# Performance work log

Measured on AMD Instinct MI355X. Metric: run time of the kernel, lower is better.

Reference implementation:

```python
import jax, jax.numpy as jnp
import numpy as np
from jax import lax

B = 8192
NUM_EXPERTS = 5
TOP_K = 3
NUM_CLASSES = 10
FEAT = 5 * 5 * 64  # 1600, flatten dim after conv stack on 28x28x1


def _conv(x, w, b):
    # NHWC input, HWIO kernel, VALID padding, stride 1
    y = lax.conv_general_dilated(x, w, (1, 1), 'VALID',
                                 dimension_numbers=('NHWC', 'HWIO', 'NHWC'))
    return y + b


def _maxpool2(x):
    return lax.reduce_window(x, -jnp.inf, lax.max,
                             (1, 2, 2, 1), (1, 2, 2, 1), 'VALID')


def setup_inputs() -> dict:
    key = jax.random.key(0)
    ks = jax.random.split(key, 8)
    x = jax.random.normal(ks[0], (B, 28, 28, 1), dtype=jnp.float32)
    # conv kernels: glorot-ish small init
    conv1_w = jax.random.normal(ks[1], (3, 3, 1, 32), dtype=jnp.float32) * 0.1
    conv1_b = jnp.zeros((32,), jnp.float32)
    conv2_w = jax.random.normal(ks[2], (3, 3, 32, 64), dtype=jnp.float32) * 0.05
    conv2_b = jnp.zeros((64,), jnp.float32)
    # gating + experts use RandomNormal(stddev=0.001), zero bias per source
    gate_w = jax.random.normal(ks[3], (FEAT, NUM_EXPERTS), dtype=jnp.float32) * 0.001
    gate_b = jnp.zeros((NUM_EXPERTS,), jnp.float32)
    exp_w = jax.random.normal(ks[4], (NUM_EXPERTS, FEAT, NUM_CLASSES), dtype=jnp.float32) * 0.001
    exp_b = jnp.zeros((NUM_EXPERTS, NUM_CLASSES), jnp.float32)
    return {'x': x, 'conv1_w': conv1_w, 'conv1_b': conv1_b,
            'conv2_w': conv2_w, 'conv2_b': conv2_b,
            'gate_w': gate_w, 'gate_b': gate_b,
            'exp_w': exp_w, 'exp_b': exp_b}


def reference(x, conv1_w, conv1_b, conv2_w, conv2_b, gate_w, gate_b, exp_w, exp_b):
    # conv backbone (dropout is identity at inference)
    h = jax.nn.relu(_conv(x, conv1_w, conv1_b))        # [B,26,26,32]
    h = _maxpool2(h)                                   # [B,13,13,32]
    h = jax.nn.relu(_conv(h, conv2_w, conv2_b))        # [B,11,11,64]
    h = _maxpool2(h)                                   # [B,5,5,64]
    feat = h.reshape(h.shape[0], -1)                   # [B,1600]

    # gating: softmax over experts, then top-k
    gates = jax.nn.softmax(feat @ gate_w + gate_b)     # [B,E]
    top_w, top_idx = lax.top_k(gates, TOP_K)           # [B,K], [B,K]

    # all-expert outputs (E small), gather the selected ones, weighted combine
    all_out = jnp.einsum('bd,edh->beh', feat, exp_w) + exp_b   # [B,E,C]
    top_out = jnp.take_along_axis(all_out, top_idx[:, :, None], axis=1)  # [B,K,C]
    combined = jnp.einsum('bkh,bk->bh', top_out, top_w)        # [B,C]

    return jax.nn.softmax(combined)
```

## Files before the change

kernel.cpp:

```cpp
#include <hip/hip_runtime.h>
#include <hip/hip_bf16.h>

#define BLOCK 512
#define IPB 4
#define EIPB 16
#define FB_STRIDE 1616
#define ES_STRIDE 1608
#define H1_STRIDE 40

#define W2T_OFF 0
#define EWT_OFF 18432
#define W1C_OFF 120832
#define WS_SHORTS 121856
#define FEAT_OFF 121856

typedef __attribute__((ext_vector_type(8))) short short8;
typedef __attribute__((ext_vector_type(4))) float f32x4;

#define SEL_LO 0x05040100u
#define SEL_HI 0x07060302u

static __device__ __forceinline__ unsigned short f2bf(float f) {
    unsigned int u = __builtin_bit_cast(unsigned int, f);
    u = (u + 0x7FFFu + ((u >> 16) & 1u)) >> 16;
    return (unsigned short)u;
}
static __device__ __forceinline__ float bf2f(unsigned short h) {
    unsigned int u = ((unsigned int)h) << 16;
    return __builtin_bit_cast(float, u);
}
static __device__ __forceinline__ unsigned int pack_hl(float v) {
    const unsigned short h = f2bf(v);
    const unsigned short l = f2bf(v - bf2f(h));
    return (unsigned int)h | ((unsigned int)l << 16);
}
static __device__ __forceinline__ unsigned int pkbf2(float a, float b) {
    return (unsigned int)f2bf(a) | ((unsigned int)f2bf(b) << 16);
}

__global__ void moe_prep(const float* __restrict__ w2, const float* __restrict__ gw,
                         const float* __restrict__ ew, const float* __restrict__ w1,
                         unsigned short* __restrict__ ws) {
    int i = blockIdx.x * 256 + threadIdx.x;
    if (i < 18432) {
        int kpos = i >> 11, rem = i & 2047, oc = rem >> 5, j = rem & 31;
        int ic = ((j & 1) << 4) | (j >> 1);
        ws[W2T_OFF + i] = f2bf(w2[(kpos * 32 + ic) * 64 + oc]);
    }
    int j2 = i - EWT_OFF;
    if (j2 >= 0 && j2 < 102400) {
        int ks = j2 >> 11, rem = j2 & 2047, n = rem >> 5, k = rem & 31;
        int kk = ks * 32 + k;
        int wv = kk >> 6, jj = kk & 63;
        int r = jj & 31;
        int oc = ((jj >> 5) << 5) | ((r & 1) << 4) | (r >> 1);
        int d = wv * 64 + oc;
        float v = 0.f;
        if (n < 50)      v = ew[(n / 10) * 16000 + d * 10 + (n % 10)];
        else if (n < 55) v = gw[d * 5 + (n - 50)];
        ws[EWT_OFF + j2] = f2bf(v);
    }
    int p = i - W1C_OFF;
    if (p >= 0 && p < 1024) {
        int n = p >> 5, k = p & 31;
        unsigned short val = 0;
        if (k < 27) {
            int t = (k < 9) ? k : (k < 18 ? k - 9 : k - 18);
            float w = w1[t * 32 + n];
            unsigned short hi = f2bf(w);
            val = (k >= 9 && k < 18) ? f2bf(w - bf2f(hi)) : hi;
        }
        ws[W1C_OFF + p] = val;
    }
}

__global__ __launch_bounds__(BLOCK, 4)
void moe_conv(const float* __restrict__ x, const float* __restrict__ b1,
              const float* __restrict__ b2, const unsigned short* __restrict__ ws,
              unsigned short* __restrict__ feat, int B)
{
    __shared__ unsigned int xsp[2][784];
    __shared__ __align__(16) unsigned short h1p[2][169 * H1_STRIDE];
    __shared__ float b1s[32];
    __shared__ float b2s[64];

    const int tid  = threadIdx.x;
    const int wid  = tid >> 6;
    const int lane = tid & 63;
    const int l15  = lane & 15;
    const int lg   = lane >> 4;

    if (tid < 32) b1s[tid] = b1[tid];
    if (tid < 64) b2s[tid] = b2[tid];

    const int mt0 = wid >> 1;
    const int n0  = (wid & 1) * 2;
    short8 bfA[9], bfB[9];
    #pragma unroll
    for (int kp = 0; kp < 9; kp++) {
        bfA[kp] = *(const short8*)&ws[W2T_OFF + (kp * 64 + n0 * 16 + l15) * 32 + lg * 8];
        bfB[kp] = *(const short8*)&ws[W2T_OFF + (kp * 64 + (n0 + 1) * 16 + l15) * 32 + lg * 8];
    }
    const short8 c1f0 = *(const short8*)&ws[W1C_OFF + l15 * 32 + lg * 8];
    const short8 c1f1 = *(const short8*)&ws[W1C_OFF + (16 + l15) * 32 + lg * 8];

    const int img0 = blockIdx.x * IPB;
    {
        int im = img0 < B ? img0 : B - 1;
        const float* xg = x + (size_t)im * 784;
        xsp[0][tid] = pack_hl(xg[tid]);
        if (tid + BLOCK < 784) xsp[0][tid + BLOCK] = pack_hl(xg[tid + BLOCK]);
    }
    __syncthreads();

    #pragma unroll
    for (int p = 0; p <= IPB; ++p) {
        const bool do_c1 = (p < IPB);
        const bool do_c2 = (p >= 1);
        const bool pre   = (p + 1 < IPB);

        float f0 = 0.f, f1 = 0.f;
        if (pre) {
            int im2 = img0 + p + 1; if (im2 >= B) im2 = B - 1;
            const float* xg2 = x + (size_t)im2 * 784;
            f0 = xg2[tid];
            if (tid + BLOCK < 784) f1 = xg2[tid + BLOCK];
        }

        if (do_c2) {
            const int it = p - 1;
            const int img = img0 + it;
            const unsigned short* h1cur = h1p[it & 1];
            unsigned short* frow = feat + (size_t)img * 1600;
            #pragma unroll
            for (int mi = 0; mi < 2; ++mi) {
                const int mt = mt0 + mi * 4;
                const int m = mt * 16 + l15;
                int wsrc = m >> 2; if (wsrc > 24) wsrc = 24;
                const int s = m & 3;
                const int cy = 2 * (wsrc / 5) + (s >> 1);
                const int cx = 2 * (wsrc % 5) + (s & 1);
                const char* abase = (const char*)h1cur + (cy * 13 + cx) * (H1_STRIDE * 2) + lg * 16;
                f32x4 a0 = {0.f, 0.f, 0.f, 0.f};
                f32x4 a1 = {0.f, 0.f, 0.f, 0.f};
                #pragma unroll
                for (int ky = 0; ky < 3; ky++) {
                    #pragma unroll
                    for (int kx = 0; kx < 3; kx++) {
                        const short8 af = *(const short8*)(abase + (ky * 13 + kx) * (H1_STRIDE * 2));
                        a0 = __builtin_amdgcn_mfma_f32_16x16x32_bf16(af, bfA[ky * 3 + kx], a0, 0, 0, 0);
                        a1 = __builtin_amdgcn_mfma_f32_16x16x32_bf16(af, bfB[ky * 3 + kx], a1, 0, 0, 0);
                    }
                }
                const int wv = mt * 4 + lg;
                if (wv < 25 && img < B) {
                    const int oc0 = n0 * 16 + l15;
                    const float m0 = fmaxf(fmaxf(a0.x, a0.y), fmaxf(a0.z, a0.w)) + b2s[oc0];
                    const float m1 = fmaxf(fmaxf(a1.x, a1.y), fmaxf(a1.z, a1.w)) + b2s[oc0 + 16];
                    *(unsigned int*)&frow[wv * 64 + ((n0 >> 1) << 5) + 2 * l15] =
                        pkbf2(fmaxf(m0, 0.f), fmaxf(m1, 0.f));
                }
            }
        }

        if (do_c1) {
            const unsigned int* xcur = xsp[p & 1];
            unsigned short* h1dst = h1p[p & 1];
            for (int mt = wid; mt < 43; mt += 8) {
                int wsrc = mt * 4 + (l15 >> 2); if (wsrc > 168) wsrc = 168;
                const int s  = l15 & 3;
                const int cy = 2 * (wsrc / 13) + (s >> 1);
                const int cx = 2 * (wsrc % 13) + (s & 1);
                const unsigned int* xb = &xcur[cy * 28 + cx];
                const unsigned int t0 = xb[0],  t1 = xb[1],  t2 = xb[2];
                const unsigned int t3 = xb[28], t4 = xb[29], t5 = xb[30];
                const unsigned int t6 = xb[56], t7 = xb[57], t8 = xb[58];
                unsigned int a0, a1, a2, a3;
                if (lg == 0)      { a0 = __builtin_amdgcn_perm(t1, t0, SEL_LO);
                                    a1 = __builtin_amdgcn_perm(t3, t2, SEL_LO);
                                    a2 = __builtin_amdgcn_perm(t5, t4, SEL_LO);
                                    a3 = __builtin_amdgcn_perm(t7, t6, SEL_LO); }
                else if (lg == 1) { a0 = __builtin_amdgcn_perm(t0, t8, SEL_LO);
                                    a1 = __builtin_amdgcn_perm(t2, t1, SEL_LO);
                                    a2 = __builtin_amdgcn_perm(t4, t3, SEL_LO);
                                    a3 = __builtin_amdgcn_perm(t6, t5, SEL_LO); }
                else if (lg == 2) { a0 = __builtin_amdgcn_perm(t8, t7, SEL_LO);
                                    a1 = __builtin_amdgcn_perm(t1, t0, SEL_HI);
                                    a2 = __builtin_amdgcn_perm(t3, t2, SEL_HI);
                                    a3 = __builtin_amdgcn_perm(t5, t4, SEL_HI); }
                else              { a0 = __builtin_amdgcn_perm(t7, t6, SEL_HI);
                                    a1 = (t8 >> 16); a2 = 0u; a3 = 0u; }
                const uint4 av = make_uint4(a0, a1, a2, a3);
                const short8 af = __builtin_bit_cast(short8, av);
                f32x4 p0 = {0.f, 0.f, 0.f, 0.f};
                f32x4 p1 = {0.f, 0.f, 0.f, 0.f};
                p0 = __builtin_amdgcn_mfma_f32_16x16x32_bf16(af, c1f0, p0, 0, 0, 0);
                p1 = __builtin_amdgcn_mfma_f32_16x16x32_bf16(af, c1f1, p1, 0, 0, 0);
                const int window = mt * 4 + lg;
                if (window < 169) {
                    const float m0 = fmaxf(fmaxf(p0.x, p0.y), fmaxf(p0.z, p0.w)) + b1s[l15];
                    const float m1 = fmaxf(fmaxf(p1.x, p1.y), fmaxf(p1.z, p1.w)) + b1s[16 + l15];
                    *(unsigned int*)&h1dst[window * H1_STRIDE + 2 * l15] =
                        pkbf2(fmaxf(m0, 0.f), fmaxf(m1, 0.f));
                }
            }
        }

        if (pre) {
            xsp[(p + 1) & 1][tid] = pack_hl(f0);
            if (tid + BLOCK < 784) xsp[(p + 1) & 1][tid + BLOCK] = pack_hl(f1);
        }
        __syncthreads();
    }
}

__global__ __launch_bounds__(BLOCK, 2)
void moe_expert(const unsigned short* __restrict__ ws, const float* __restrict__ gb,
                const float* __restrict__ eb, float* __restrict__ out, int B)
{
    __shared__ __align__(16) unsigned short featS[EIPB * ES_STRIDE];
    __shared__ float allC[2][EIPB][64];

    const int tid  = threadIdx.x;
    const int wid  = tid >> 6;
    const int lane = tid & 63;
    const int l15  = lane & 15;
    const int lg   = lane >> 4;

    const unsigned short* feat = ws + FEAT_OFF;
    const unsigned short* ewt  = ws + EWT_OFF;
    const int img0 = blockIdx.x * EIPB;

    for (int i = tid; i < EIPB * 800; i += BLOCK) {
        const int r = i / 800, c = i - r * 800;
        const int img = img0 + r;
        unsigned int v = 0u;
        if (img < B) v = *(const unsigned int*)&feat[(size_t)img * 1600 + 2 * c];
        *(unsigned int*)&featS[r * ES_STRIDE + 2 * c] = v;
    }
    __syncthreads();

    {
        const int kh  = wid >> 2;
        const int ntE = wid & 3;
        const int bc  = ntE * 16 + l15;
        f32x4 acc = {0.f, 0.f, 0.f, 0.f};
        const int ks0 = kh * 25;
        for (int ks = ks0; ks < ks0 + 25; ++ks) {
            const short8 af = *(const short8*)&featS[l15 * ES_STRIDE + ks * 32 + lg * 8];
            const short8 bf = *(const short8*)&ewt[(ks * 64 + bc) * 32 + lg * 8];
            acc = __builtin_amdgcn_mfma_f32_16x16x32_bf16(af, bf, acc, 0, 0, 0);
        }
        const int r0 = lg * 4;
        allC[kh][r0 + 0][bc] = acc.x;
        allC[kh][r0 + 1][bc] = acc.y;
        allC[kh][r0 + 2][bc] = acc.z;
        allC[kh][r0 + 3][bc] = acc.w;
    }
    __syncthreads();

    if (tid < EIPB) {
        const int img = img0 + tid;
        if (img < B) {
            float gv[5], mx = -1e30f;
            #pragma unroll
            for (int g = 0; g < 5; g++) {
                gv[g] = allC[0][tid][50 + g] + allC[1][tid][50 + g] + gb[g];
                mx = fmaxf(mx, gv[g]);
            }
            float ssum = 0.f;
            #pragma unroll
            for (int g = 0; g < 5; g++) { gv[g] = expf(gv[g] - mx); ssum += gv[g]; }
            const float inv = 1.f / ssum;
            #pragma unroll
            for (int g = 0; g < 5; g++) gv[g] *= inv;

            int idx0, idx1, idx2; float wv0, wv1, wv2;
            unsigned usedMask = 0;
            {
                int bi = 0; float bv = -1e30f;
                #pragma unroll
                for (int g = 0; g < 5; g++)
                    if (gv[g] > bv) { bv = gv[g]; bi = g; }
                idx0 = bi; wv0 = bv; usedMask |= (1u << bi);
            }
            {
                int bi = 0; float bv = -1e30f;
                #pragma unroll
                for (int g = 0; g < 5; g++)
                    if (!(usedMask & (1u << g)) && gv[g] > bv) { bv = gv[g]; bi = g; }
                idx1 = bi; wv1 = bv; usedMask |= (1u << bi);
            }
            {
                int bi = 0; float bv = -1e30f;
                #pragma unroll
                for (int g = 0; g < 5; g++)
                    if (!(usedMask & (1u << g)) && gv[g] > bv) { bv = gv[g]; bi = g; }
                idx2 = bi; wv2 = bv;
            }
            float comb[10];
            #pragma unroll
            for (int cc = 0; cc < 10; cc++) {
                comb[cc] = wv0 * (allC[0][tid][idx0 * 10 + cc] + allC[1][tid][idx0 * 10 + cc] + eb[idx0 * 10 + cc])
                         + wv1 * (allC[0][tid][idx1 * 10 + cc] + allC[1][tid][idx1 * 10 + cc] + eb[idx1 * 10 + cc])
                         + wv2 * (allC[0][tid][idx2 * 10 + cc] + allC[1][tid][idx2 * 10 + cc] + eb[idx2 * 10 + cc]);
            }
            float m2 = -1e30f;
            #pragma unroll
            for (int cc = 0; cc < 10; cc++) m2 = fmaxf(m2, comb[cc]);
            float e[10], s2 = 0.f;
            #pragma unroll
            for (int cc = 0; cc < 10; cc++) { e[cc] = expf(comb[cc] - m2); s2 += e[cc]; }
            const float inv2 = 1.f / s2;
            #pragma unroll
            for (int cc = 0; cc < 10; cc++) out[(size_t)img * 10 + cc] = e[cc] * inv2;
        }
    }
}

__global__ __launch_bounds__(BLOCK, 3)
void moe_main_fused(const float* __restrict__ x, const float* __restrict__ b1,
                    const float* __restrict__ b2, const float* __restrict__ gb,
                    const float* __restrict__ eb, const unsigned short* __restrict__ ws,
                    float* __restrict__ out, int B)
{
    __shared__ unsigned int xsp[2][784];
    __shared__ __align__(16) unsigned short h1p[2][169 * H1_STRIDE];
    __shared__ __align__(16) unsigned short featbuf[IPB * FB_STRIDE];
    __shared__ float b1s[32];
    __shared__ float b2s[64];
    __shared__ float allC[2][IPB * 56];

    const int tid  = threadIdx.x;
    const int wid  = tid >> 6;
    const int lane = tid & 63;
    const int l15  = lane & 15;
    const int lg   = lane >> 4;

    if (tid < 32) b1s[tid] = b1[tid];
    if (tid < 64) b2s[tid] = b2[tid];

    const int mt0 = wid >> 1;
    const int n0  = (wid & 1) * 2;
    short8 bfA[9], bfB[9];
    #pragma unroll
    for (int kp = 0; kp < 9; kp++) {
        bfA[kp] = *(const short8*)&ws[W2T_OFF + (kp * 64 + n0 * 16 + l15) * 32 + lg * 8];
        bfB[kp] = *(const short8*)&ws[W2T_OFF + (kp * 64 + (n0 + 1) * 16 + l15) * 32 + lg * 8];
    }
    const short8 c1f0 = *(const short8*)&ws[W1C_OFF + l15 * 32 + lg * 8];
    const short8 c1f1 = *(const short8*)&ws[W1C_OFF + (16 + l15) * 32 + lg * 8];

    const int img0 = blockIdx.x * IPB;
    {
        int im = img0 < B ? img0 : B - 1;
        const float* xg = x + (size_t)im * 784;
        xsp[0][tid] = pack_hl(xg[tid]);
        if (tid + BLOCK < 784) xsp[0][tid + BLOCK] = pack_hl(xg[tid + BLOCK]);
    }
    __syncthreads();

    #pragma unroll
    for (int p = 0; p <= IPB; ++p) {
        const bool do_c1 = (p < IPB);
        const bool do_c2 = (p >= 1);
        const bool pre   = (p + 1 < IPB);

        float f0 = 0.f, f1 = 0.f;
        if (pre) {
            int im2 = img0 + p + 1; if (im2 >= B) im2 = B - 1;
            const float* xg2 = x + (size_t)im2 * 784;
            f0 = xg2[tid];
            if (tid + BLOCK < 784) f1 = xg2[tid + BLOCK];
        }

        if (do_c2) {
            const int it = p - 1;
            const unsigned short* h1cur = h1p[it & 1];
            #pragma unroll
            for (int mi = 0; mi < 2; ++mi) {
                const int mt = mt0 + mi * 4;
                const int m = mt * 16 + l15;
                int wsrc = m >> 2; if (wsrc > 24) wsrc = 24;
                const int s = m & 3;
                const int cy = 2 * (wsrc / 5) + (s >> 1);
                const int cx = 2 * (wsrc % 5) + (s & 1);
                const char* abase = (const char*)h1cur + (cy * 13 + cx) * (H1_STRIDE * 2) + lg * 16;
                f32x4 a0 = {0.f, 0.f, 0.f, 0.f};
                f32x4 a1 = {0.f, 0.f, 0.f, 0.f};
                #pragma unroll
                for (int ky = 0; ky < 3; ky++) {
                    #pragma unroll
                    for (int kx = 0; kx < 3; kx++) {
                        const short8 af = *(const short8*)(abase + (ky * 13 + kx) * (H1_STRIDE * 2));
                        a0 = __builtin_amdgcn_mfma_f32_16x16x32_bf16(af, bfA[ky * 3 + kx], a0, 0, 0, 0);
                        a1 = __builtin_amdgcn_mfma_f32_16x16x32_bf16(af, bfB[ky * 3 + kx], a1, 0, 0, 0);
                    }
                }
                const int wv = mt * 4 + lg;
                if (wv < 25) {
                    const int oc0 = n0 * 16 + l15;
                    const float m0 = fmaxf(fmaxf(a0.x, a0.y), fmaxf(a0.z, a0.w)) + b2s[oc0];
                    const float m1 = fmaxf(fmaxf(a1.x, a1.y), fmaxf(a1.z, a1.w)) + b2s[oc0 + 16];
                    *(unsigned int*)&featbuf[it * FB_STRIDE + wv * 64 + ((n0 >> 1) << 5) + 2 * l15] =
                        pkbf2(fmaxf(m0, 0.f), fmaxf(m1, 0.f));
                }
            }
        }

        if (do_c1) {
            const unsigned int* xcur = xsp[p & 1];
            unsigned short* h1dst = h1p[p & 1];
            for (int mt = wid; mt < 43; mt += 8) {
                int wsrc = mt * 4 + (l15 >> 2); if (wsrc > 168) wsrc = 168;
                const int s  = l15 & 3;
                const int cy = 2 * (wsrc / 13) + (s >> 1);
                const int cx = 2 * (wsrc % 13) + (s & 1);
                const unsigned int* xb = &xcur[cy * 28 + cx];
                const unsigned int t0 = xb[0],  t1 = xb[1],  t2 = xb[2];
                const unsigned int t3 = xb[28], t4 = xb[29], t5 = xb[30];
                const unsigned int t6 = xb[56], t7 = xb[57], t8 = xb[58];
                unsigned int a0, a1, a2, a3;
                if (lg == 0)      { a0 = __builtin_amdgcn_perm(t1, t0, SEL_LO);
                                    a1 = __builtin_amdgcn_perm(t3, t2, SEL_LO);
                                    a2 = __builtin_amdgcn_perm(t5, t4, SEL_LO);
                                    a3 = __builtin_amdgcn_perm(t7, t6, SEL_LO); }
                else if (lg == 1) { a0 = __builtin_amdgcn_perm(t0, t8, SEL_LO);
                                    a1 = __builtin_amdgcn_perm(t2, t1, SEL_LO);
                                    a2 = __builtin_amdgcn_perm(t4, t3, SEL_LO);
                                    a3 = __builtin_amdgcn_perm(t6, t5, SEL_LO); }
                else if (lg == 2) { a0 = __builtin_amdgcn_perm(t8, t7, SEL_LO);
                                    a1 = __builtin_amdgcn_perm(t1, t0, SEL_HI);
                                    a2 = __builtin_amdgcn_perm(t3, t2, SEL_HI);
                                    a3 = __builtin_amdgcn_perm(t5, t4, SEL_HI); }
                else              { a0 = __builtin_amdgcn_perm(t7, t6, SEL_HI);
                                    a1 = (t8 >> 16); a2 = 0u; a3 = 0u; }
                const uint4 av = make_uint4(a0, a1, a2, a3);
                const short8 af = __builtin_bit_cast(short8, av);
                f32x4 p0 = {0.f, 0.f, 0.f, 0.f};
                f32x4 p1 = {0.f, 0.f, 0.f, 0.f};
                p0 = __builtin_amdgcn_mfma_f32_16x16x32_bf16(af, c1f0, p0, 0, 0, 0);
                p1 = __builtin_amdgcn_mfma_f32_16x16x32_bf16(af, c1f1, p1, 0, 0, 0);
                const int window = mt * 4 + lg;
                if (window < 169) {
                    const float m0 = fmaxf(fmaxf(p0.x, p0.y), fmaxf(p0.z, p0.w)) + b1s[l15];
                    const float m1 = fmaxf(fmaxf(p1.x, p1.y), fmaxf(p1.z, p1.w)) + b1s[16 + l15];
                    *(unsigned int*)&h1dst[window * H1_STRIDE + 2 * l15] =
                        pkbf2(fmaxf(m0, 0.f), fmaxf(m1, 0.f));
                }
            }
        }

        if (pre) {
            xsp[(p + 1) & 1][tid] = pack_hl(f0);
            if (tid + BLOCK < 784) xsp[(p + 1) & 1][tid + BLOCK] = pack_hl(f1);
        }
        __syncthreads();
    }

    {
        const unsigned short* ewt = ws + EWT_OFF;
        const int kh = wid >> 2;
        const int ntE = wid & 3;
        const int bc = ntE * 16 + l15;
        const int arow = l15 & (IPB - 1);
        f32x4 acc = {0.f, 0.f, 0.f, 0.f};
        const int ks0 = kh * 25;
        for (int ks = ks0; ks < ks0 + 25; ++ks) {
            const short8 af = *(const short8*)&featbuf[arow * FB_STRIDE + ks * 32 + lg * 8];
            const short8 bf = *(const short8*)&ewt[(ks * 64 + bc) * 32 + lg * 8];
            acc = __builtin_amdgcn_mfma_f32_16x16x32_bf16(af, bf, acc, 0, 0, 0);
        }
        if (lane < 16 && bc < 56) {
            allC[kh][0 * 56 + bc] = acc.x;
            allC[kh][1 * 56 + bc] = acc.y;
            allC[kh][2 * 56 + bc] = acc.z;
            allC[kh][3 * 56 + bc] = acc.w;
        }
    }
    __syncthreads();

    if (tid < IPB) {
        const int img = img0 + tid;
        if (img < B) {
            float gv[5], mx = -1e30f;
            #pragma unroll
            for (int g = 0; g < 5; g++) {
                gv[g] = allC[0][tid * 56 + 50 + g] + allC[1][tid * 56 + 50 + g] + gb[g];
                mx = fmaxf(mx, gv[g]);
            }
            float ssum = 0.f;
            #pragma unroll
            for (int g = 0; g < 5; g++) { gv[g] = expf(gv[g] - mx); ssum += gv[g]; }
            const float inv = 1.f / ssum;
            #pragma unroll
            for (int g = 0; g < 5; g++) gv[g] *= inv;

            int idx0, idx1, idx2; float wv0, wv1, wv2;
            unsigned usedMask = 0;
            {
                int bi = 0; float bv = -1e30f;
                #pragma unroll
                for (int g = 0; g < 5; g++)
                    if (gv[g] > bv) { bv = gv[g]; bi = g; }
                idx0 = bi; wv0 = bv; usedMask |= (1u << bi);
            }
            {
                int bi = 0; float bv = -1e30f;
                #pragma unroll
                for (int g = 0; g < 5; g++)
                    if (!(usedMask & (1u << g)) && gv[g] > bv) { bv = gv[g]; bi = g; }
                idx1 = bi; wv1 = bv; usedMask |= (1u << bi);
            }
            {
                int bi = 0; float bv = -1e30f;
                #pragma unroll
                for (int g = 0; g < 5; g++)
                    if (!(usedMask & (1u << g)) && gv[g] > bv) { bv = gv[g]; bi = g; }
                idx2 = bi; wv2 = bv;
            }
            float comb[10];
            #pragma unroll
            for (int cc = 0; cc < 10; cc++) {
                comb[cc] = wv0 * (allC[0][tid * 56 + idx0 * 10 + cc] + allC[1][tid * 56 + idx0 * 10 + cc] + eb[idx0 * 10 + cc])
                         + wv1 * (allC[0][tid * 56 + idx1 * 10 + cc] + allC[1][tid * 56 + idx1 * 10 + cc] + eb[idx1 * 10 + cc])
                         + wv2 * (allC[0][tid * 56 + idx2 * 10 + cc] + allC[1][tid * 56 + idx2 * 10 + cc] + eb[idx2 * 10 + cc]);
            }
            float m2 = -1e30f;
            #pragma unroll
            for (int cc = 0; cc < 10; cc++) m2 = fmaxf(m2, comb[cc]);
            float e[10], s2 = 0.f;
            #pragma unroll
            for (int cc = 0; cc < 10; cc++) { e[cc] = expf(comb[cc] - m2); s2 += e[cc]; }
            const float inv2 = 1.f / s2;
            #pragma unroll
            for (int cc = 0; cc < 10; cc++) out[(size_t)img * 10 + cc] = e[cc] * inv2;
        }
    }
}

extern "C" void kernel_launch(void* const* d_in, const int* in_sizes, int n_in,
                              void* d_out, int out_size, void* d_ws, size_t ws_size,
                              hipStream_t stream) {
    const float* x   = (const float*)d_in[0];
    const float* w1  = (const float*)d_in[1];
    const float* b1  = (const float*)d_in[2];
    const float* w2  = (const float*)d_in[3];
    const float* b2  = (const float*)d_in[4];
    const float* gw  = (const float*)d_in[5];
    const float* gb  = (const float*)d_in[6];
    const float* ew  = (const float*)d_in[7];
    const float* eb  = (const float*)d_in[8];
    float* out = (float*)d_out;
    const int B = in_sizes[0] / 784;

    unsigned short* ws = (unsigned short*)d_ws;
    const size_t ws_full = ((size_t)WS_SHORTS + (size_t)B * 1600) * sizeof(unsigned short);

    moe_prep<<<(WS_SHORTS + 255) / 256, 256, 0, stream>>>(w2, gw, ew, w1, ws);
    if (ws_size >= ws_full) {
        moe_conv<<<(B + IPB - 1) / IPB, BLOCK, 0, stream>>>(x, b1, b2, ws, ws + FEAT_OFF, B);
        moe_expert<<<(B + EIPB - 1) / EIPB, BLOCK, 0, stream>>>(ws, gb, eb, out, B);
    } else {
        moe_main_fused<<<(B + IPB - 1) / IPB, BLOCK, 0, stream>>>(x, b1, b2, gb, eb, ws, out, B);
    }
}
```

Before: 97.99 us.

## Drop low-bf16 split for conv1 input, batch more images per conv block

The conv1 input is now packed as plain bf16 with the hardware v_cvt_pk_bf16_f32 instruction. The hi/lo split that fed the x-residual terms into conv1 is removed, so the MFMA operand and the weight layout each lose one K segment. IPB is doubled to 8 images per conv block, launch bounds drop to 3, and the per-lane conv1/conv2 address offsets are precomputed outside the image loop. This cuts ALU work per image and spreads the weight-register loading over more images, at the cost of lower input precision in conv1 and possibly lower occupancy.

```diff
diff --git a/kernel.cpp b/kernel.cpp
--- a/kernel.cpp
+++ b/kernel.cpp
@@ -2,7 +2,7 @@
 #include <hip/hip_bf16.h>
 
 #define BLOCK 512
-#define IPB 4
+#define IPB 8
 #define EIPB 16
 #define FB_STRIDE 1616
 #define ES_STRIDE 1608
@@ -29,13 +29,10 @@
     unsigned int u = ((unsigned int)h) << 16;
     return __builtin_bit_cast(float, u);
 }
-static __device__ __forceinline__ unsigned int pack_hl(float v) {
-    const unsigned short h = f2bf(v);
-    const unsigned short l = f2bf(v - bf2f(h));
-    return (unsigned int)h | ((unsigned int)l << 16);
-}
-static __device__ __forceinline__ unsigned int pkbf2(float a, float b) {
-    return (unsigned int)f2bf(a) | ((unsigned int)f2bf(b) << 16);
+static __device__ __forceinline__ unsigned int cvtpk(float a, float b) {
+    unsigned int r;
+    asm("v_cvt_pk_bf16_f32 %0, %1, %2" : "=v"(r) : "v"(a), "v"(b));
+    return r;
 }
 
 __global__ void moe_prep(const float* __restrict__ w2, const float* __restrict__ gw,
@@ -64,17 +61,17 @@
     if (p >= 0 && p < 1024) {
         int n = p >> 5, k = p & 31;
         unsigned short val = 0;
-        if (k < 27) {
-            int t = (k < 9) ? k : (k < 18 ? k - 9 : k - 18);
+        if (k < 18) {
+            int t = (k < 9) ? k : k - 9;
             float w = w1[t * 32 + n];
             unsigned short hi = f2bf(w);
-            val = (k >= 9 && k < 18) ? f2bf(w - bf2f(hi)) : hi;
+            val = (k >= 9) ? f2bf(w - bf2f(hi)) : hi;
         }
         ws[W1C_OFF + p] = val;
     }
 }
 
-__global__ __launch_bounds__(BLOCK, 4)
+__global__ __launch_bounds__(BLOCK, 3)
 void moe_conv(const float* __restrict__ x, const float* __restrict__ b1,
               const float* __restrict__ b2, const unsigned short* __restrict__ ws,
               unsigned short* __restrict__ feat, int B)
@@ -104,12 +101,42 @@
     const short8 c1f0 = *(const short8*)&ws[W1C_OFF + l15 * 32 + lg * 8];
     const short8 c1f1 = *(const short8*)&ws[W1C_OFF + (16 + l15) * 32 + lg * 8];
 
+    int xoff1[6], hoff1[6];
+    bool val1[6];
+    #pragma unroll
+    for (int j = 0; j < 6; ++j) {
+        const int mt = wid + 8 * j;
+        int wsrc = mt * 4 + (l15 >> 2); if (wsrc > 168) wsrc = 168;
+        const int s = l15 & 3;
+        const int cy = 2 * (wsrc / 13) + (s >> 1);
+        const int cx = 2 * (wsrc % 13) + (s & 1);
+        xoff1[j] = cy * 28 + cx;
+        const int window = mt * 4 + lg;
+        val1[j] = (mt < 43) && (window < 169);
+        hoff1[j] = (window < 169 ? window : 0) * H1_STRIDE + 2 * l15;
+    }
+    int aoff2[2], foff2[2];
+    bool val2[2];
+    #pragma unroll
+    for (int mi = 0; mi < 2; ++mi) {
+        const int mt = mt0 + mi * 4;
+        const int m = mt * 16 + l15;
+        int wsrc = m >> 2; if (wsrc > 24) wsrc = 24;
+        const int s = m & 3;
+        const int cy = 2 * (wsrc / 5) + (s >> 1);
+        const int cx = 2 * (wsrc % 5) + (s & 1);
+        aoff2[mi] = (cy * 13 + cx) * (H1_STRIDE * 2) + lg * 16;
+        const int wv = mt * 4 + lg;
+        val2[mi] = (wv < 25);
+        foff2[mi] = (wv < 25 ? wv : 0) * 64 + ((n0 >> 1) << 5) + 2 * l15;
+    }
+
     const int img0 = blockIdx.x * IPB;
     {
         int im = img0 < B ? img0 : B - 1;
         const float* xg = x + (size_t)im * 784;
-        xsp[0][tid] = pack_hl(xg[tid]);
-        if (tid + BLOCK < 784) xsp[0][tid + BLOCK] = pack_hl(xg[tid + BLOCK]);
+        xsp[0][tid] = cvtpk(xg[tid], xg[tid]);
+        if (tid + BLOCK < 784) xsp[0][tid + BLOCK] = cvtpk(xg[tid + BLOCK], xg[tid + BLOCK]);
     }
     __syncthreads();
 
@@ -132,6 +159,235 @@
             const int img = img0 + it;
             const unsigned short* h1cur = h1p[it & 1];
             unsigned short* frow = feat + (size_t)img * 1600;
+            #pragma unroll
+            for (int mi = 0; mi < 2; ++mi) {
+                const char* abase = (const char*)h1cur + aoff2[mi];
+                f32x4 a0 = {0.f, 0.f, 0.f, 0.f};
+                f32x4 a1 = {0.f, 0.f, 0.f, 0.f};
+                #pragma unroll
+                for (int kp = 0; kp < 9; kp++) {
+                    const int ky = kp / 3, kx = kp % 3;
+                    const short8 af = *(const short8*)(abase + (ky * 13 + kx) * (H1_STRIDE * 2));
+                    a0 = __builtin_amdgcn_mfma_f32_16x16x32_bf16(af, bfA[kp], a0, 0, 0, 0);
+                    a1 = __builtin_amdgcn_mfma_f32_16x16x32_bf16(af, bfB[kp], a1, 0, 0, 0);
+                }
+                if (val2[mi] && img < B) {
+                    const int oc0 = n0 * 16 + l15;
+                    const float m0 = fmaxf(fmaxf(a0.x, a0.y), fmaxf(a0.z, a0.w)) + b2s[oc0];
+                    const float m1 = fmaxf(fmaxf(a1.x, a1.y), fmaxf(a1.z, a1.w)) + b2s[oc0 + 16];
+                    *(unsigned int*)&frow[foff2[mi]] = cvtpk(fmaxf(m0, 0.f), fmaxf(m1, 0.f));
+                }
+            }
+        }
+
+        if (do_c1) {
+            const unsigned int* xcur = xsp[p & 1];
+            unsigned short* h1dst = h1p[p & 1];
+            #pragma unroll
+            for (int j = 0; j < 6; ++j) {
+                if (wid + 8 * j < 43) {
+                    const unsigned int* xb = xcur + xoff1[j];
+                    const unsigned int t0 = xb[0],  t1 = xb[1],  t2 = xb[2];
+                    const unsigned int t3 = xb[28], t4 = xb[29], t5 = xb[30];
+                    const unsigned int t6 = xb[56], t7 = xb[57], t8 = xb[58];
+                    unsigned int a0, a1, a2, a3;
+                    if (lg == 0)      { a0 = __builtin_amdgcn_perm(t1, t0, SEL_LO);
+                                        a1 = __builtin_amdgcn_perm(t3, t2, SEL_LO);
+                                        a2 = __builtin_amdgcn_perm(t5, t4, SEL_LO);
+                                        a3 = __builtin_amdgcn_perm(t7, t6, SEL_LO); }
+                    else if (lg == 1) { a0 = __builtin_amdgcn_perm(t0, t8, SEL_LO);
+                                        a1 = __builtin_amdgcn_perm(t2, t1, SEL_LO);
+                                        a2 = __builtin_amdgcn_perm(t4, t3, SEL_LO);
+                                        a3 = __builtin_amdgcn_perm(t6, t5, SEL_LO); }
+                    else if (lg == 2) { a0 = __builtin_amdgcn_perm(t8, t7, SEL_LO);
+                                        a1 = 0u; a2 = 0u; a3 = 0u; }
+                    else              { a0 = 0u; a1 = 0u; a2 = 0u; a3 = 0u; }
+                    const uint4 av = make_uint4(a0, a1, a2, a3);
+                    const short8 af = __builtin_bit_cast(short8, av);
+                    f32x4 p0 = {0.f, 0.f, 0.f, 0.f};
+                    f32x4 p1 = {0.f, 0.f, 0.f, 0.f};
+                    p0 = __builtin_amdgcn_mfma_f32_16x16x32_bf16(af, c1f0, p0, 0, 0, 0);
+                    p1 = __builtin_amdgcn_mfma_f32_16x16x32_bf16(af, c1f1, p1, 0, 0, 0);
+                    if (val1[j]) {
+                        const float m0 = fmaxf(fmaxf(p0.x, p0.y), fmaxf(p0.z, p0.w)) + b1s[l15];
+                        const float m1 = fmaxf(fmaxf(p1.x, p1.y), fmaxf(p1.z, p1.w)) + b1s[16 + l15];
+                        *(unsigned int*)&h1dst[hoff1[j]] = cvtpk(fmaxf(m0, 0.f), fmaxf(m1, 0.f));
+                    }
+                }
+            }
+        }
+
+        if (pre) {
+            xsp[(p + 1) & 1][tid] = cvtpk(f0, f0);
+            if (tid + BLOCK < 784) xsp[(p + 1) & 1][tid + BLOCK] = cvtpk(f1, f1);
+        }
+        __syncthreads();
+    }
+}
+
+__global__ __launch_bounds__(BLOCK, 2)
+void moe_expert(const unsigned short* __restrict__ ws, const float* __restrict__ gb,
+                const float* __restrict__ eb, float* __restrict__ out, int B)
+{
+    __shared__ __align__(16) unsigned short featS[EIPB * ES_STRIDE];
+    __shared__ float allC[2][EIPB][64];
+
+    const int tid  = threadIdx.x;
+    const int wid  = tid >> 6;
+    const int lane = tid & 63;
+    const int l15  = lane & 15;
+    const int lg   = lane >> 4;
+
+    const unsigned short* feat = ws + FEAT_OFF;
+    const unsigned short* ewt  = ws + EWT_OFF;
+    const int img0 = blockIdx.x * EIPB;
+
+    for (int i = tid; i < EIPB * 800; i += BLOCK) {
+        const int r = i / 800, c = i - r * 800;
+        const int img = img0 + r;
+        unsigned int v = 0u;
+        if (img < B) v = *(const unsigned int*)&feat[(size_t)img * 1600 + 2 * c];
+        *(unsigned int*)&featS[r * ES_STRIDE + 2 * c] = v;
+    }
+    __syncthreads();
+
+    {
+        const int kh  = wid >> 2;
+        const int ntE = wid & 3;
+        const int bc  = ntE * 16 + l15;
+        f32x4 acc = {0.f, 0.f, 0.f, 0.f};
+        const int ks0 = kh * 25;
+        for (int ks = ks0; ks < ks0 + 25; ++ks) {
+            const short8 af = *(const short8*)&featS[l15 * ES_STRIDE + ks * 32 + lg * 8];
+            const short8 bf = *(const short8*)&ewt[(ks * 64 + bc) * 32 + lg * 8];
+            acc = __builtin_amdgcn_mfma_f32_16x16x32_bf16(af, bf, acc, 0, 0, 0);
+        }
+        const int r0 = lg * 4;
+        allC[kh][r0 + 0][bc] = acc.x;
+        allC[kh][r0 + 1][bc] = acc.y;
+        allC[kh][r0 + 2][bc] = acc.z;
+        allC[kh][r0 + 3][bc] = acc.w;
+    }
+    __syncthreads();
+
+    if (tid < EIPB) {
+        const int img = img0 + tid;
+        if (img < B) {
+            float gv[5], mx = -1e30f;
+            #pragma unroll
+            for (int g = 0; g < 5; g++) {
+                gv[g] = allC[0][tid][50 + g] + allC[1][tid][50 + g] + gb[g];
+                mx = fmaxf(mx, gv[g]);
+            }
+            float ssum = 0.f;
+            #pragma unroll
+            for (int g = 0; g < 5; g++) { gv[g] = expf(gv[g] - mx); ssum += gv[g]; }
+            const float inv = 1.f / ssum;
+            #pragma unroll
+            for (int g = 0; g < 5; g++) gv[g] *= inv;
+
+            int idx0, idx1, idx2; float wv0, wv1, wv2;
+            unsigned usedMask = 0;
+            {
+                int bi = 0; float bv = -1e30f;
+                #pragma unroll
+                for (int g = 0; g < 5; g++)
+                    if (gv[g] > bv) { bv = gv[g]; bi = g; }
+                idx0 = bi; wv0 = bv; usedMask |= (1u << bi);
+            }
+            {
+                int bi = 0; float bv = -1e30f;
+                #pragma unroll
+                for (int g = 0; g < 5; g++)
+                    if (!(usedMask & (1u << g)) && gv[g] > bv) { bv = gv[g]; bi = g; }
+                idx1 = bi; wv1 = bv; usedMask |= (1u << bi);
+            }
+            {
+                int bi = 0; float bv = -1e30f;
+                #pragma unroll
+                for (int g = 0; g < 5; g++)
+                    if (!(usedMask & (1u << g)) && gv[g] > bv) { bv = gv[g]; bi = g; }
+                idx2 = bi; wv2 = bv;
+            }
+            float comb[10];
+            #pragma unroll
+            for (int cc = 0; cc < 10; cc++) {
+                comb[cc] = wv0 * (allC[0][tid][idx0 * 10 + cc] + allC[1][tid][idx0 * 10 + cc] + eb[idx0 * 10 + cc])
+                         + wv1 * (allC[0][tid][idx1 * 10 + cc] + allC[1][tid][idx1 * 10 + cc] + eb[idx1 * 10 + cc])
+                         + wv2 * (allC[0][tid][idx2 * 10 + cc] + allC[1][tid][idx2 * 10 + cc] + eb[idx2 * 10 + cc]);
+            }
+            float m2 = -1e30f;
+            #pragma unroll
+            for (int cc = 0; cc < 10; cc++) m2 = fmaxf(m2, comb[cc]);
+            float e[10], s2 = 0.f;
+            #pragma unroll
+            for (int cc = 0; cc < 10; cc++) { e[cc] = expf(comb[cc] - m2); s2 += e[cc]; }
+            const float inv2 = 1.f / s2;
+            #pragma unroll
+            for (int cc = 0; cc < 10; cc++) out[(size_t)img * 10 + cc] = e[cc] * inv2;
+        }
+    }
+}
+
+__global__ __launch_bounds__(BLOCK, 3)
+void moe_main_fused(const float* __restrict__ x, const float* __restrict__ b1,
+                    const float* __restrict__ b2, const float* __restrict__ gb,
+                    const float* __restrict__ eb, const unsigned short* __restrict__ ws,
+                    float* __restrict__ out, int B)
+{
+    __shared__ unsigned int xsp[2][784];
+    __shared__ __align__(16) unsigned short h1p[2][169 * H1_STRIDE];
+    __shared__ __align__(16) unsigned short featbuf[4 * FB_STRIDE];
+    __shared__ float b1s[32];
+    __shared__ float b2s[64];
+    __shared__ float allC[2][4 * 56];
+
+    const int tid  = threadIdx.x;
+    const int wid  = tid >> 6;
+    const int lane = tid & 63;
+    const int l15  = lane & 15;
+    const int lg   = lane >> 4;
+
+    if (tid < 32) b1s[tid] = b1[tid];
+    if (tid < 64) b2s[tid] = b2[tid];
+
+    const int mt0 = wid >> 1;
+    const int n0  = (wid & 1) * 2;
+    short8 bfA[9], bfB[9];
+    #pragma unroll
+    for (int kp = 0; kp < 9; kp++) {
+        bfA[kp] = *(const short8*)&ws[W2T_OFF + (kp * 64 + n0 * 16 + l15) * 32 + lg * 8];
+        bfB[kp] = *(const short8*)&ws[W2T_OFF + (kp * 64 + (n0 + 1) * 16 + l15) * 32 + lg * 8];
+    }
+    const short8 c1f0 = *(const short8*)&ws[W1C_OFF + l15 * 32 + lg * 8];
+    const short8 c1f1 = *(const short8*)&ws[W1C_OFF + (16 + l15) * 32 + lg * 8];
+
+    const int img0 = blockIdx.x * 4;
+    {
+        int im = img0 < B ? img0 : B - 1;
+        const float* xg = x + (size_t)im * 784;
+        xsp[0][tid] = cvtpk(xg[tid], xg[tid]);
+        if (tid + BLOCK < 784) xsp[0][tid + BLOCK] = cvtpk(xg[tid + BLOCK], xg[tid + BLOCK]);
+    }
+    __syncthreads();
+
+    #pragma unroll
+    for (int p = 0; p <= 4; ++p) {
+        const bool do_c1 = (p < 4);
+        const bool do_c2 = (p >= 1);
+        const bool pre   = (p + 1 < 4);
+
+        float f0 = 0.f, f1 = 0.f;
+        if (pre) {
+            int im2 = img0 + p + 1; if (im2 >= B) im2 = B - 1;
+            const float* xg2 = x + (size_t)im2 * 784;
+            f0 = xg2[tid];
+            if (tid + BLOCK < 784) f1 = xg2[tid + BLOCK];
+        }
+
+        if (do_c2) {
+            const int it = p - 1;
+            const unsigned short* h1cur = h1p[it & 1];
             #pragma unroll
             for (int mi = 0; mi < 2; ++mi) {
                 const int mt = mt0 + mi * 4;
@@ -144,21 +400,19 @@
                 f32x4 a0 = {0.f, 0.f, 0.f, 0.f};
                 f32x4 a1 = {0.f, 0.f, 0.f, 0.f};
                 #pragma unroll
-                for (int ky = 0; ky < 3; ky++) {
-                    #pragma unroll
-                    for (int kx = 0; kx < 3; kx++) {
-                        const short8 af = *(const short8*)(abase + (ky * 13 + kx) * (H1_STRIDE * 2));
-                        a0 = __builtin_amdgcn_mfma_f32_16x16x32_bf16(af, bfA[ky * 3 + kx], a0, 0, 0, 0);
-                        a1 = __builtin_amdgcn_mfma_f32_16x16x32_bf16(af, bfB[ky * 3 + kx], a1, 0, 0, 0);
-                    }
+                for (int kp = 0; kp < 9; kp++) {
+                    const int ky = kp / 3, kx = kp % 3;
+                    const short8 af = *(const short8*)(abase + (ky * 13 + kx) * (H1_STRIDE * 2));
+                    a0 = __builtin_amdgcn_mfma_f32_16x16x32_bf16(af, bfA[kp], a0, 0, 0, 0);
+                    a1 = __builtin_amdgcn_mfma_f32_16x16x32_bf16(af, bfB[kp], a1, 0, 0, 0);
                 }
                 const int wv = mt * 4 + lg;
-                if (wv < 25 && img < B) {
+                if (wv < 25) {
                     const int oc0 = n0 * 16 + l15;
                     const float m0 = fmaxf(fmaxf(a0.x, a0.y), fmaxf(a0.z, a0.w)) + b2s[oc0];
                     const float m1 = fmaxf(fmaxf(a1.x, a1.y), fmaxf(a1.z, a1.w)) + b2s[oc0 + 16];
-                    *(unsigned int*)&frow[wv * 64 + ((n0 >> 1) << 5) + 2 * l15] =
-                        pkbf2(fmaxf(m0, 0.f), fmaxf(m1, 0.f));
+                    *(unsigned int*)&featbuf[it * FB_STRIDE + wv * 64 + ((n0 >> 1) << 5) + 2 * l15] =
+                        cvtpk(fmaxf(m0, 0.f), fmaxf(m1, 0.f));
                 }
             }
         }
@@ -185,11 +439,8 @@
                                     a2 = __builtin_amdgcn_perm(t4, t3, SEL_LO);
                                     a3 = __builtin_amdgcn_perm(t6, t5, SEL_LO); }
                 else if (lg == 2) { a0 = __builtin_amdgcn_perm(t8, t7, SEL_LO);
-                                    a1 = __builtin_amdgcn_perm(t1, t0, SEL_HI);
-                                    a2 = __builtin_amdgcn_perm(t3, t2, SEL_HI);
-                                    a3 = __builtin_amdgcn_perm(t5, t4, SEL_HI); }
-                else              { a0 = __builtin_amdgcn_perm(t7, t6, SEL_HI);
-                                    a1 = (t8 >> 16); a2 = 0u; a3 = 0u; }
+                                    a1 = 0u; a2 = 0u; a3 = 0u; }
+                else              { a0 = 0u; a1 = 0u; a2 = 0u; a3 = 0u; }
                 const uint4 av = make_uint4(a0, a1, a2, a3);
                 const short8 af = __builtin_bit_cast(short8, av);
                 f32x4 p0 = {0.f, 0.f, 0.f, 0.f};
@@ -201,259 +452,14 @@
                     const float m0 = fmaxf(fmaxf(p0.x, p0.y), fmaxf(p0.z, p0.w)) + b1s[l15];
                     const float m1 = fmaxf(fmaxf(p1.x, p1.y), fmaxf(p1.z, p1.w)) + b1s[16 + l15];
                     *(unsigned int*)&h1dst[window * H1_STRIDE + 2 * l15] =
-                        pkbf2(fmaxf(m0, 0.f), fmaxf(m1, 0.f));
+                        cvtpk(fmaxf(m0, 0.f), fmaxf(m1, 0.f));
                 }
             }
         }
 
         if (pre) {
-            xsp[(p + 1) & 1][tid] = pack_hl(f0);
-            if (tid + BLOCK < 784) xsp[(p + 1) & 1][tid + BLOCK] = pack_hl(f1);
-        }
-        __syncthreads();
-    }
-}
-
-__global__ __launch_bounds__(BLOCK, 2)
-void moe_expert(const unsigned short* __restrict__ ws, const float* __restrict__ gb,
-                const float* __restrict__ eb, float* __restrict__ out, int B)
-{
-    __shared__ __align__(16) unsigned short featS[EIPB * ES_STRIDE];
-    __shared__ float allC[2][EIPB][64];
-
-    const int tid  = threadIdx.x;
-    const int wid  = tid >> 6;
-    const int lane = tid & 63;
-    const int l15  = lane & 15;
-    const int lg   = lane >> 4;
-
-    const unsigned short* feat = ws + FEAT_OFF;
-    const unsigned short* ewt  = ws + EWT_OFF;
-    const int img0 = blockIdx.x * EIPB;
-
-    for (int i = tid; i < EIPB * 800; i += BLOCK) {
-        const int r = i / 800, c = i - r * 800;
-        const int img = img0 + r;
-        unsigned int v = 0u;
-        if (img < B) v = *(const unsigned int*)&feat[(size_t)img * 1600 + 2 * c];
-        *(unsigned int*)&featS[r * ES_STRIDE + 2 * c] = v;
-    }
-    __syncthreads();
-
-    {
-        const int kh  = wid >> 2;
-        const int ntE = wid & 3;
-        const int bc  = ntE * 16 + l15;
-        f32x4 acc = {0.f, 0.f, 0.f, 0.f};
-        const int ks0 = kh * 25;
-        for (int ks = ks0; ks < ks0 + 25; ++ks) {
-            const short8 af = *(const short8*)&featS[l15 * ES_STRIDE + ks * 32 + lg * 8];
-            const short8 bf = *(const short8*)&ewt[(ks * 64 + bc) * 32 + lg * 8];
-            acc = __builtin_amdgcn_mfma_f32_16x16x32_bf16(af, bf, acc, 0, 0, 0);
-        }
-        const int r0 = lg * 4;
-        allC[kh][r0 + 0][bc] = acc.x;
-        allC[kh][r0 + 1][bc] = acc.y;
-        allC[kh][r0 + 2][bc] = acc.z;
-        allC[kh][r0 + 3][bc] = acc.w;
-    }
-    __syncthreads();
-
-    if (tid < EIPB) {
-        const int img = img0 + tid;
-        if (img < B) {
-            float gv[5], mx = -1e30f;
-            #pragma unroll
-            for (int g = 0; g < 5; g++) {
-                gv[g] = allC[0][tid][50 + g] + allC[1][tid][50 + g] + gb[g];
-                mx = fmaxf(mx, gv[g]);
-            }
-            float ssum = 0.f;
-            #pragma unroll
-            for (int g = 0; g < 5; g++) { gv[g] = expf(gv[g] - mx); ssum += gv[g]; }
-            const float inv = 1.f / ssum;
-            #pragma unroll
-            for (int g = 0; g < 5; g++) gv[g] *= inv;
-
-            int idx0, idx1, idx2; float wv0, wv1, wv2;
-            unsigned usedMask = 0;
-            {
-                int bi = 0; float bv = -1e30f;
-                #pragma unroll
-                for (int g = 0; g < 5; g++)
-                    if (gv[g] > bv) { bv = gv[g]; bi = g; }
-                idx0 = bi; wv0 = bv; usedMask |= (1u << bi);
-            }
-            {
-                int bi = 0; float bv = -1e30f;
-                #pragma unroll
-                for (int g = 0; g < 5; g++)
-                    if (!(usedMask & (1u << g)) && gv[g] > bv) { bv = gv[g]; bi = g; }
-                idx1 = bi; wv1 = bv; usedMask |= (1u << bi);
-            }
-            {
-                int bi = 0; float bv = -1e30f;
-                #pragma unroll
-                for (int g = 0; g < 5; g++)
-                    if (!(usedMask & (1u << g)) && gv[g] > bv) { bv = gv[g]; bi = g; }
-                idx2 = bi; wv2 = bv;
-            }
-            float comb[10];
-            #pragma unroll
-            for (int cc = 0; cc < 10; cc++) {
-                comb[cc] = wv0 * (allC[0][tid][idx0 * 10 + cc] + allC[1][tid][idx0 * 10 + cc] + eb[idx0 * 10 + cc])
-                         + wv1 * (allC[0][tid][idx1 * 10 + cc] + allC[1][tid][idx1 * 10 + cc] + eb[idx1 * 10 + cc])
-                         + wv2 * (allC[0][tid][idx2 * 10 + cc] + allC[1][tid][idx2 * 10 + cc] + eb[idx2 * 10 + cc]);
-            }
-            float m2 = -1e30f;
-            #pragma unroll
-            for (int cc = 0; cc < 10; cc++) m2 = fmaxf(m2, comb[cc]);
-            float e[10], s2 = 0.f;
-            #pragma unroll
-            for (int cc = 0; cc < 10; cc++) { e[cc] = expf(comb[cc] - m2); s2 += e[cc]; }
-            const float inv2 = 1.f / s2;
-            #pragma unroll
-            for (int cc = 0; cc < 10; cc++) out[(size_t)img * 10 + cc] = e[cc] * inv2;
-        }
-    }
-}
-
-__global__ __launch_bounds__(BLOCK, 3)
-void moe_main_fused(const float* __restrict__ x, const float* __restrict__ b1,
-                    const float* __restrict__ b2, const float* __restrict__ gb,
-                    const float* __restrict__ eb, const unsigned short* __restrict__ ws,
-                    float* __restrict__ out, int B)
-{
-    __shared__ unsigned int xsp[2][784];
-    __shared__ __align__(16) unsigned short h1p[2][169 * H1_STRIDE];
-    __shared__ __align__(16) unsigned short featbuf[IPB * FB_STRIDE];
-    __shared__ float b1s[32];
-    __shared__ float b2s[64];
-    __shared__ float allC[2][IPB * 56];
-
-    const int tid  = threadIdx.x;
-    const int wid  = tid >> 6;
-    const int lane = tid & 63;
-    const int l15  = lane & 15;
-    const int lg   = lane >> 4;
-
-    if (tid < 32) b1s[tid] = b1[tid];
-    if (tid < 64) b2s[tid] = b2[tid];
-
-    const int mt0 = wid >> 1;
-    const int n0  = (wid & 1) * 2;
-    short8 bfA[9], bfB[9];
-    #pragma unroll
-    for (int kp = 0; kp < 9; kp++) {
-        bfA[kp] = *(const short8*)&ws[W2T_OFF + (kp * 64 + n0 * 16 + l15) * 32 + lg * 8];
-        bfB[kp] = *(const short8*)&ws[W2T_OFF + (kp * 64 + (n0 + 1) * 16 + l15) * 32 + lg * 8];
-    }
-    const short8 c1f0 = *(const short8*)&ws[W1C_OFF + l15 * 32 + lg * 8];
-    const short8 c1f1 = *(const short8*)&ws[W1C_OFF + (16 + l15) * 32 + lg * 8];
-
-    const int img0 = blockIdx.x * IPB;
-    {
-        int im = img0 < B ? img0 : B - 1;
-        const float* xg = x + (size_t)im * 784;
-        xsp[0][tid] = pack_hl(xg[tid]);
-        if (tid + BLOCK < 784) xsp[0][tid + BLOCK] = pack_hl(xg[tid + BLOCK]);
-    }
-    __syncthreads();
-
-    #pragma unroll
-    for (int p = 0; p <= IPB; ++p) {
-        const bool do_c1 = (p < IPB);
-        const bool do_c2 = (p >= 1);
-        const bool pre   = (p + 1 < IPB);
-
-        float f0 = 0.f, f1 = 0.f;
-        if (pre) {
-            int im2 = img0 + p + 1; if (im2 >= B) im2 = B - 1;
-            const float* xg2 = x + (size_t)im2 * 784;
-            f0 = xg2[tid];
-            if (tid + BLOCK < 784) f1 = xg2[tid + BLOCK];
-        }
-
-        if (do_c2) {
-            const int it = p - 1;
-            const unsigned short* h1cur = h1p[it & 1];
-            #pragma unroll
-            for (int mi = 0; mi < 2; ++mi) {
-                const int mt = mt0 + mi * 4;
-                const int m = mt * 16 + l15;
-                int wsrc = m >> 2; if (wsrc > 24) wsrc = 24;
-                const int s = m & 3;
-                const int cy = 2 * (wsrc / 5) + (s >> 1);
-                const int cx = 2 * (wsrc % 5) + (s & 1);
-                const char* abase = (const char*)h1cur + (cy * 13 + cx) * (H1_STRIDE * 2) + lg * 16;
-                f32x4 a0 = {0.f, 0.f, 0.f, 0.f};
-                f32x4 a1 = {0.f, 0.f, 0.f, 0.f};
-                #pragma unroll
-                for (int ky = 0; ky < 3; ky++) {
-                    #pragma unroll
-                    for (int kx = 0; kx < 3; kx++) {
-                        const short8 af = *(const short8*)(abase + (ky * 13 + kx) * (H1_STRIDE * 2));
-                        a0 = __builtin_amdgcn_mfma_f32_16x16x32_bf16(af, bfA[ky * 3 + kx], a0, 0, 0, 0);
-                        a1 = __builtin_amdgcn_mfma_f32_16x16x32_bf16(af, bfB[ky * 3 + kx], a1, 0, 0, 0);
-                    }
-                }
-                const int wv = mt * 4 + lg;
-                if (wv < 25) {
-                    const int oc0 = n0 * 16 + l15;
-                    const float m0 = fmaxf(fmaxf(a0.x, a0.y), fmaxf(a0.z, a0.w)) + b2s[oc0];
-                    const float m1 = fmaxf(fmaxf(a1.x, a1.y), fmaxf(a1.z, a1.w)) + b2s[oc0 + 16];
-                    *(unsigned int*)&featbuf[it * FB_STRIDE + wv * 64 + ((n0 >> 1) << 5) + 2 * l15] =
-                        pkbf2(fmaxf(m0, 0.f), fmaxf(m1, 0.f));
-                }
-            }
-        }
-
-        if (do_c1) {
-            const unsigned int* xcur = xsp[p & 1];
-            unsigned short* h1dst = h1p[p & 1];
-            for (int mt = wid; mt < 43; mt += 8) {
-                int wsrc = mt * 4 + (l15 >> 2); if (wsrc > 168) wsrc = 168;
-                const int s  = l15 & 3;
-                const int cy = 2 * (wsrc / 13) + (s >> 1);
-                const int cx = 2 * (wsrc % 13) + (s & 1);
-                const unsigned int* xb = &xcur[cy * 28 + cx];
-                const unsigned int t0 = xb[0],  t1 = xb[1],  t2 = xb[2];
-                const unsigned int t3 = xb[28], t4 = xb[29], t5 = xb[30];
-                const unsigned int t6 = xb[56], t7 = xb[57], t8 = xb[58];
-                unsigned int a0, a1, a2, a3;
-                if (lg == 0)      { a0 = __builtin_amdgcn_perm(t1, t0, SEL_LO);
-                                    a1 = __builtin_amdgcn_perm(t3, t2, SEL_LO);
-                                    a2 = __builtin_amdgcn_perm(t5, t4, SEL_LO);
-                                    a3 = __builtin_amdgcn_perm(t7, t6, SEL_LO); }
-                else if (lg == 1) { a0 = __builtin_amdgcn_perm(t0, t8, SEL_LO);
-                                    a1 = __builtin_amdgcn_perm(t2, t1, SEL_LO);
-                                    a2 = __builtin_amdgcn_perm(t4, t3, SEL_LO);
-                                    a3 = __builtin_amdgcn_perm(t6, t5, SEL_LO); }
-                else if (lg == 2) { a0 = __builtin_amdgcn_perm(t8, t7, SEL_LO);
-                                    a1 = __builtin_amdgcn_perm(t1, t0, SEL_HI);
-                                    a2 = __builtin_amdgcn_perm(t3, t2, SEL_HI);
-                                    a3 = __builtin_amdgcn_perm(t5, t4, SEL_HI); }
-                else              { a0 = __builtin_amdgcn_perm(t7, t6, SEL_HI);
-                                    a1 = (t8 >> 16); a2 = 0u; a3 = 0u; }
-                const uint4 av = make_uint4(a0, a1, a2, a3);
-                const short8 af = __builtin_bit_cast(short8, av);
-                f32x4 p0 = {0.f, 0.f, 0.f, 0.f};
-                f32x4 p1 = {0.f, 0.f, 0.f, 0.f};
-                p0 = __builtin_amdgcn_mfma_f32_16x16x32_bf16(af, c1f0, p0, 0, 0, 0);
-                p1 = __builtin_amdgcn_mfma_f32_16x16x32_bf16(af, c1f1, p1, 0, 0, 0);
-                const int window = mt * 4 + lg;
-                if (window < 169) {
-                    const float m0 = fmaxf(fmaxf(p0.x, p0.y), fmaxf(p0.z, p0.w)) + b1s[l15];
-                    const float m1 = fmaxf(fmaxf(p1.x, p1.y), fmaxf(p1.z, p1.w)) + b1s[16 + l15];
-                    *(unsigned int*)&h1dst[window * H1_STRIDE + 2 * l15] =
-                        pkbf2(fmaxf(m0, 0.f), fmaxf(m1, 0.f));
-                }
-            }
-        }
-
-        if (pre) {
-            xsp[(p + 1) & 1][tid] = pack_hl(f0);
-            if (tid + BLOCK < 784) xsp[(p + 1) & 1][tid + BLOCK] = pack_hl(f1);
+            xsp[(p + 1) & 1][tid] = cvtpk(f0, f0);
+            if (tid + BLOCK < 784) xsp[(p + 1) & 1][tid + BLOCK] = cvtpk(f1, f1);
         }
         __syncthreads();
     }
@@ -463,7 +469,7 @@
         const int kh = wid >> 2;
         const int ntE = wid & 3;
         const int bc = ntE * 16 + l15;
-        const int arow = l15 & (IPB - 1);
+        const int arow = l15 & 3;
         f32x4 acc = {0.f, 0.f, 0.f, 0.f};
         const int ks0 = kh * 25;
         for (int ks = ks0; ks < ks0 + 25; ++ks) {
@@ -480,7 +486,7 @@
     }
     __syncthreads();
 
-    if (tid < IPB) {
+    if (tid < 4) {
         const int img = img0 + tid;
         if (img < B) {
             float gv[5], mx = -1e30f;
@@ -562,6 +568,6 @@
         moe_conv<<<(B + IPB - 1) / IPB, BLOCK, 0, stream>>>(x, b1, b2, ws, ws + FEAT_OFF, B);
         moe_expert<<<(B + EIPB - 1) / EIPB, BLOCK, 0, stream>>>(ws, gb, eb, out, B);
     } else {
-        moe_main_fused<<<(B + IPB - 1) / IPB, BLOCK, 0, stream>>>(x, b1, b2, gb, eb, ws, out, B);
-    }
-}
+        moe_main_fused<<<(B + 3) / 4, BLOCK, 0, stream>>>(x, b1, b2, gb, eb, ws, out, B);
+    }
+}
```

New measurement: 81.36 us. -17.0%, faster.
